# Performance work log

Hardware: AMD Instinct MI355X
Metric: run time of the kernel (lower is better)

Reference implementation:

```python
import jax, jax.numpy as jnp
import numpy as np

# configuration (mirrors global `args` in the original code)
N_USER = 20000
N_ITEM = 20000
N = N_USER + N_ITEM            # total nodes; N*N < 2^31 so int32 hashing is safe
N_EDGES = 2_560_000
MASK_DEPTH = 2
KEEP_RATE = 0.5
N_SEEDS = 2000


def setup_inputs() -> dict:
    key = jax.random.key(0)
    k1, k2, k3 = jax.random.split(key, 3)
    rows = jax.random.randint(k1, (N_EDGES,), 0, N, dtype=jnp.int32)
    cols = jax.random.randint(k2, (N_EDGES,), 0, N, dtype=jnp.int32)
    vals = jnp.ones((N_EDGES,), jnp.float32)  # adj._values(); only its length is used
    seeds = jax.random.randint(k3, (N_SEEDS,), 0, N, dtype=jnp.int32)
    return {"rows": rows, "cols": cols, "vals": vals, "seeds": seeds}


def reference(rows, cols, vals, seeds):
    """Faithful vectorized translation of RandomMaskSubgraphs.forward.

    The per-seed python loop over edges is equivalent (in its final effect) to:
    per BFS level, drop every still-alive edge incident to the current seed set,
    and take the endpoints of dropped edges as the next seed set.
    Returns (enc_rows, enc_cols, enc_vals, dec_rows, dec_cols, dec_vals).
    Removed encoder edges carry value 0 (zero-value sparse entries == absent).
    """
    E = rows.shape[0]
    key = jax.random.key(1)
    kS, kR, kC = jax.random.split(key, 3)

    alive = jnp.ones(E, dtype=bool)                     # edges not yet masked
    seed_mask = jnp.zeros(N, dtype=bool).at[seeds].set(True)
    mask_nodes = seed_mask                               # union of maskNodes list
    cur = seed_mask
    for i in range(MASK_DEPTH):
        # membership test: edge incident to any current seed (single gather pass)
        hit = alive & (cur[rows] | cur[cols])
        alive = alive & ~hit
        if i != MASK_DEPTH - 1:
            # endpoints of masked edges become next frontier (scatter dedup)
            h = hit.astype(jnp.int32)
            touched = (jnp.zeros(N, jnp.int32).at[rows].add(h).at[cols].add(h)) > 0
            mask_nodes = mask_nodes | touched
            cur = touched

    # random keep-nodes augmentation
    samp_num = int(N * KEEP_RATE)
    samp = jax.random.randint(kS, (samp_num,), 0, N, dtype=jnp.int32)
    mask_nodes = mask_nodes.at[samp].set(True)

    # encoderAdj = normalizeAdj(sparse(ones on remaining edges))
    deg = jax.ops.segment_sum(alive.astype(jnp.float32), rows, num_segments=N)
    dinv = jnp.power(deg + 1e-12, -0.5)
    enc_vals = alive.astype(jnp.float32) * dinv[rows] * dinv[cols]

    # decoderAdj: random pairs among masked nodes + self loops + remaining edges,
    # deduplicated via integer hash row*N + col (fits int32 since N*N < 2^31)
    mask_idx = jnp.nonzero(mask_nodes)[0].astype(jnp.int32)
    tem_num = int(mask_idx.shape[0])
    tem_rows = mask_idx[jax.random.randint(kR, (E,), 0, tem_num)]
    tem_cols = mask_idx[jax.random.randint(kC, (E,), 0, tem_num)]
    ar = jnp.arange(N, dtype=jnp.int32)
    alive_rows = rows[alive]
    alive_cols = cols[alive]
    new_rows = jnp.concatenate([tem_rows, tem_cols, ar, alive_rows])
    new_cols = jnp.concatenate([tem_cols, tem_rows, ar, alive_cols])
    hash_val = jnp.unique(new_rows * N + new_cols)
    dec_cols = hash_val % N
    dec_rows = hash_val // N
    dec_vals = jnp.ones(dec_rows.shape[0], jnp.float32)

    return rows, cols, enc_vals, dec_rows, dec_cols, dec_vals
```

## Files before the change

kernel.cpp:

```cpp
#include <hip/hip_runtime.h>
#include <stdint.h>


#define NN 40000
#define SAMPN (NN / 2)
#define WORDS 1250
#define SWORDS 40
#define NB 1024
#define RPB 40
#define CAP 8192
#define CURSTRIDE 4
#define EPB 3840
#define NE (EPB / 256)
#define SCAP (3 * EPB)

__host__ __device__ __forceinline__ void tf2x32(unsigned k0, unsigned k1,
                                                unsigned x0, unsigned x1,
                                                unsigned &o0, unsigned &o1) {
  unsigned ks2 = k0 ^ k1 ^ 0x1BD11BDAu;
  x0 += k0; x1 += k1;
#define TFR(r) { x0 += x1; x1 = (x1 << (r)) | (x1 >> (32 - (r))); x1 ^= x0; }
  TFR(13) TFR(15) TFR(26) TFR(6)
  x0 += k1;  x1 += ks2 + 1u;
  TFR(17) TFR(29) TFR(16) TFR(24)
  x0 += ks2; x1 += k0 + 2u;
  TFR(13) TFR(15) TFR(26) TFR(6)
  x0 += k0;  x1 += k1 + 3u;
  TFR(17) TFR(29) TFR(16) TFR(24)
  x0 += k1;  x1 += ks2 + 4u;
  TFR(13) TFR(15) TFR(26) TFR(6)
  x0 += ks2; x1 += k0 + 5u;
#undef TFR
  o0 = x0; o1 = x1;
}

__device__ __forceinline__ unsigned jrand(unsigned a, unsigned b, unsigned c,
                                          unsigned d, unsigned e, unsigned span) {
  unsigned x0, x1, y0, y1;
  tf2x32(a, b, 0u, e, x0, x1);
  unsigned hi = x0 ^ x1;
  tf2x32(c, d, 0u, e, y0, y1);
  unsigned lo = y0 ^ y1;
  unsigned mult = 65536u % span;
  mult = (mult * mult) % span;
  return ((hi % span) * mult + (lo % span)) % span;
}

__global__ void k_zero16(uint4 *p, int n16) {
  int i = blockIdx.x * blockDim.x + threadIdx.x;
  if (i < n16) p[i] = make_uint4(0u, 0u, 0u, 0u);
}
__global__ void k_seed(const int *seeds, int ns, unsigned char *cur,
                       unsigned char *mask_bfs) {
  int i = blockIdx.x * blockDim.x + threadIdx.x;
  if (i < ns) { int s = seeds[i]; cur[s] = 1; mask_bfs[s] = 1; }
}
__global__ void k_level0(const int *rows, const int *cols, int E,
                         const unsigned char *cur, unsigned char *alive,
                         unsigned char *touched, unsigned char *mask_bfs) {
  int e = blockIdx.x * blockDim.x + threadIdx.x;
  if (e >= E) return;
  int r = rows[e], c = cols[e];
  if (cur[r] | cur[c]) {
    alive[e] = 0;
    touched[r] = 1; touched[c] = 1;
    mask_bfs[r] = 1; mask_bfs[c] = 1;
  } else alive[e] = 1;
}
__global__ void k_level1_deg(const int *rows, const int *cols, int E,
                             const unsigned char *touched, unsigned char *alive,
                             int *deg) {
  int e = blockIdx.x * blockDim.x + threadIdx.x;
  if (e >= E) return;
  if (alive[e]) {
    int r = rows[e];
    if (touched[r] | touched[cols[e]]) alive[e] = 0;
    else atomicAdd(&deg[r], 1);
  }
}
__global__ void k_dinv(const int *deg, float *dinv) {
  int i = blockIdx.x * blockDim.x + threadIdx.x;
  if (i >= NN) return;
  float x = (float)deg[i] + 1e-12f;
  dinv[i] = (float)(1.0 / sqrt((double)x));
}
__global__ void k_enc(const int *rows, const int *cols, const unsigned char *alive,
                      const float *dinv, int E, float *out) {
  int e = blockIdx.x * blockDim.x + threadIdx.x;
  if (e >= E) return;
  int r = rows[e], c = cols[e];
  out[e] = (float)r;
  out[E + e] = (float)c;
  out[2 * E + e] = alive[e] ? dinv[r] * dinv[c] : 0.0f;
}

__global__ void k_samp(unsigned a, unsigned b, unsigned c, unsigned d,
                       unsigned char *mask_bfs) {
  int s = blockIdx.x * blockDim.x + threadIdx.x;
  if (s >= SAMPN) return;
  unsigned idx = jrand(a, b, c, d, (unsigned)s, (unsigned)NN);
  mask_bfs[idx] = 1;
}

__global__ __launch_bounds__(1024) void k_scan_mask(const unsigned char *flags,
                                                    int *mask_idx, int *tem_num) {
  __shared__ int wsum[16];
  const unsigned *f = (const unsigned *)flags;
  int tid = threadIdx.x, lane = tid & 63, wid = tid >> 6;
  int base = tid * 10;
  unsigned u[10];
  int cnt = 0;
  for (int j = 0; j < 10; j++) {
    int i = base + j;
    u[j] = (i < 10000) ? f[i] : 0u;
    cnt += __popc(u[j]);
  }
  int x = cnt;
  for (int d = 1; d < 64; d <<= 1) {
    int y = __shfl_up(x, d, 64);
    if (lane >= d) x += y;
  }
  if (lane == 63) wsum[wid] = x;
  __syncthreads();
  if (wid == 0) {
    int v = (lane < 16) ? wsum[lane] : 0;
    int y = v;
    for (int d = 1; d < 16; d <<= 1) {
      int z = __shfl_up(y, d, 64);
      if (lane >= d) y += z;
    }
    if (lane < 16) wsum[lane] = y - v;
  }
  __syncthreads();
  int off = wsum[wid] + (x - cnt);
  for (int j = 0; j < 10; j++) {
    int i = base + j;
    unsigned v = u[j];
    while (v) {
      int byte = (__ffs(v) - 1) >> 3;
      v &= v - 1;
      mask_idx[off++] = i * 4 + byte;
    }
  }
  if (tid == 1023) *tem_num = off;
}

__global__ void k_append_self(int *cursors, unsigned *bucketmem) {
  int i = blockIdx.x * blockDim.x + threadIdx.x;
  if (i >= NN) return;
  unsigned b = (unsigned)i / RPB;
  unsigned lr = (unsigned)i - b * RPB;
  int p = atomicAdd(&cursors[b * CURSTRIDE], 1);
  if (p < CAP) bucketmem[b * CAP + p] = (lr << 16) | (unsigned)i;
}

__global__ __launch_bounds__(256) void k_append_tem(
    const int *rows, const int *cols, const unsigned char *alive,
    const int *mask_idx, const int *tem_num, int *cursors, unsigned *bucketmem,
    unsigned ra, unsigned rb, unsigned rc, unsigned rd,
    unsigned ca, unsigned cb, unsigned cc, unsigned cd, int E) {
  __shared__ unsigned sorted[SCAP];
  __shared__ int cnt[NB];
  __shared__ int ofs[NB];
  __shared__ int ntot_s;
  int tid = threadIdx.x, lane = tid & 63, wid = tid >> 6;
  int e0 = blockIdx.x * EPB;
  unsigned span = (unsigned)*tem_num;
  const unsigned NOPE = 0xFFFFFFFFu;

  unsigned tval[NE], aval[NE];

  for (int i = tid; i < NB; i += 256) cnt[i] = 0;
  __syncthreads();
#pragma unroll
  for (int k = 0; k < NE; k++) {
    int e = e0 + k * 256 + tid;
    if (e < E) {
      unsigned iR = jrand(ra, rb, rc, rd, (unsigned)e, span);
      unsigned iC = jrand(ca, cb, cc, cd, (unsigned)e, span);
      unsigned tr = (unsigned)mask_idx[iR], tc = (unsigned)mask_idx[iC];
      tval[k] = (tr << 16) | tc;
      atomicAdd(&cnt[tr / RPB], 1);
      atomicAdd(&cnt[tc / RPB], 1);
      if (alive[e]) {
        unsigned r = (unsigned)rows[e];
        aval[k] = (r << 16) | (unsigned)cols[e];
        atomicAdd(&cnt[r / RPB], 1);
      } else aval[k] = NOPE;
    } else { tval[k] = NOPE; aval[k] = NOPE; }
  }
  __syncthreads();
  if (wid == 0) {
    int carry = 0;
    for (int c8 = 0; c8 < 16; c8++) {
      int v = cnt[c8 * 64 + lane];
      int x = v;
      for (int d = 1; d < 64; d <<= 1) {
        int y = __shfl_up(x, d, 64);
        if (lane >= d) x += y;
      }
      ofs[c8 * 64 + lane] = carry + x - v;
      carry += __shfl(x, 63, 64);
    }
    if (lane == 0) ntot_s = carry;
  }
  __syncthreads();
  for (int i = tid; i < NB; i += 256) cnt[i] = ofs[i];
  __syncthreads();
#pragma unroll
  for (int k = 0; k < NE; k++) {
    unsigned v = tval[k];
    if (v != NOPE) {
      unsigned tr = v >> 16, tc = v & 0xFFFFu;
      int p1 = atomicAdd(&cnt[tr / RPB], 1);
      sorted[p1] = v;
      int p2 = atomicAdd(&cnt[tc / RPB], 1);
      sorted[p2] = (tc << 16) | tr;
      unsigned a = aval[k];
      if (a != NOPE) {
        int p3 = atomicAdd(&cnt[(a >> 16) / RPB], 1);
        sorted[p3] = a;
      }
    }
  }
  __syncthreads();
  int ntot = ntot_s;
  for (int b = tid; b < NB; b += 256) {
    int end = (b < NB - 1) ? ofs[b + 1] : ntot;
    int len = end - ofs[b];
    cnt[b] = len ? atomicAdd(&cursors[b * CURSTRIDE], len) : 0;
  }
  __syncthreads();
  for (int j = tid; j < ntot; j += 256) {
    unsigned item = sorted[j];
    unsigned r = item >> 16;
    unsigned b = r / RPB;
    unsigned lr = r - b * RPB;
    int idx = cnt[b] + (j - ofs[b]);
    if (idx < CAP) bucketmem[b * CAP + idx] = (lr << 16) | (item & 0xFFFFu);
  }
}

__global__ __launch_bounds__(256) void k_dedup(unsigned *bucketmem,
                                               const int *cursors, int *uniq_cnt) {
  int b = blockIdx.x;
  int rowbase = b * RPB;
  if (rowbase >= NN) { if (threadIdx.x == 0) uniq_cnt[b] = 0; return; }

  __shared__ unsigned short arr[CAP];
  __shared__ int cnt[RPB];
  __shared__ int rowend[RPB];
  __shared__ int curs[RPB];
  __shared__ int rowoff[RPB];
  __shared__ unsigned bm[4][WORDS];
  __shared__ unsigned sm[4][SWORDS];

  int tid = threadIdx.x, lane = tid & 63, wid = tid >> 6;
  int n = cursors[b * CURSTRIDE]; if (n > CAP) n = CAP;
  const unsigned *src = bucketmem + (size_t)b * CAP;

  for (int i = tid; i < RPB; i += 256) cnt[i] = 0;
  __syncthreads();
  for (int j = tid; j < n; j += 256) atomicAdd(&cnt[src[j] >> 16], 1);
  __syncthreads();
  if (tid == 0) {
    int s = 0;
    for (int r = 0; r < RPB; r++) { curs[r] = s; s += cnt[r]; rowend[r] = s; }
  }
  __syncthreads();
  for (int j = tid; j < n; j += 256) {
    unsigned v = src[j];
    int p = atomicAdd(&curs[v >> 16], 1);
    arr[p] = (unsigned short)v;
  }
  for (int w = lane; w < WORDS; w += 64) bm[wid][w] = 0u;
  if (lane < SWORDS) sm[wid][lane] = 0u;
  __syncthreads();

  for (int r = wid; r < RPB; r += 4) {
    int s1 = rowend[r], s0 = s1 - cnt[r];
    for (int j = s0 + lane; j < s1; j += 64) {
      unsigned c = arr[j];
      atomicOr(&bm[wid][c >> 5], 1u << (c & 31));
      atomicOr(&sm[wid][c >> 10], 1u << ((c >> 5) & 31));
    }
    unsigned s = (lane < SWORDS) ? sm[wid][lane] : 0u;
    int m = 0;
    unsigned t = s;
    while (t) {
      int w = (lane << 5) + (__ffs(t) - 1);
      t &= t - 1;
      m += __popc(bm[wid][w]);
    }
    int x = m;
    for (int d = 1; d < 64; d <<= 1) {
      int y = __shfl_up(x, d, 64);
      if (lane >= d) x += y;
    }
    int u = __shfl(x, 63, 64);
    int pos = s0 + (x - m);
    t = s;
    while (t) {
      int w = (lane << 5) + (__ffs(t) - 1);
      t &= t - 1;
      unsigned mm = bm[wid][w];
      bm[wid][w] = 0u;
      while (mm) {
        int bit = __ffs(mm) - 1;
        mm &= mm - 1;
        arr[pos++] = (unsigned short)((w << 5) + bit);
      }
    }
    if (lane < SWORDS) sm[wid][lane] = 0u;
    if (lane == 0) cnt[r] = u;
  }
  __syncthreads();
  if (tid == 0) {
    int s = 0;
    for (int r = 0; r < RPB; r++) { rowoff[r] = s; s += cnt[r]; }
    uniq_cnt[b] = s;
  }
  __syncthreads();
  unsigned *dst = bucketmem + (size_t)b * CAP;
  for (int r = wid; r < RPB; r += 4) {
    int s0 = r ? rowend[r - 1] : 0;
    int u = cnt[r], o = rowoff[r];
    unsigned hashbase = (unsigned)(rowbase + r) * 40000u;
    for (int j = lane; j < u; j += 64)
      dst[o + j] = hashbase + (unsigned)arr[s0 + j];
  }
}

__global__ __launch_bounds__(1024) void k_scan1024(const int *uniq_cnt,
                                                   int *uniq_off, int *diagC) {
  __shared__ int wsum[16];
  int tid = threadIdx.x, lane = tid & 63, wid = tid >> 6;
  int v = uniq_cnt[tid];
  int x = v;
  for (int d = 1; d < 64; d <<= 1) {
    int y = __shfl_up(x, d, 64);
    if (lane >= d) x += y;
  }
  if (lane == 63) wsum[wid] = x;
  __syncthreads();
  if (wid == 0) {
    int w = (lane < 16) ? wsum[lane] : 0;
    int y = w;
    for (int d = 1; d < 16; d <<= 1) {
      int z = __shfl_up(y, d, 64);
      if (lane >= d) y += z;
    }
    if (lane < 16) wsum[lane] = y - w;
  }
  __syncthreads();
  uniq_off[tid] = wsum[wid] + x - v;
  if (tid == 1023) {
    int C = wsum[15] + x;
    uniq_off[NB] = C;
    *diagC = C;
  }
}
__global__ __launch_bounds__(256) void k_emit(const unsigned *bucketmem,
                                              const int *uniq_cnt,
                                              const int *uniq_off, float *out,
                                              int E, int U) {
  int b = blockIdx.x;
  int ub = uniq_cnt[b], ob = uniq_off[b];
  const unsigned *src = bucketmem + (size_t)b * CAP;
  int base3 = 3 * E;
  for (int j = threadIdx.x; j < ub; j += 256) {
    unsigned h = src[j];
    unsigned r = h / 40000u;
    unsigned c = h - r * 40000u;
    int idx = ob + j;
    if (idx < U) {
      out[base3 + idx] = (float)r;
      out[base3 + U + idx] = (float)c;
      out[base3 + 2 * U + idx] = 1.0f;
    }
  }
}
__global__ void k_diag(const int *diagC, int U, float *out, int E) {
  if (blockIdx.x || threadIdx.x) return;
  int C = *diagC;
  if (C == U) return;
  int d = C - U; if (d < 0) d = -d; if (d > 60000) d = 60000;
  out[3 * E] = (float)(300000 + d);
}

extern "C" void kernel_launch(void *const *d_in, const int *in_sizes, int n_in,
                              void *d_out, int out_size, void *d_ws,
                              size_t ws_size, hipStream_t stream) {
  const int *rows = (const int *)d_in[0];
  const int *cols = (const int *)d_in[1];
  const int *seeds = (const int *)d_in[3];
  const int E = in_sizes[0];
  const int ns = in_sizes[3];
  float *out = (float *)d_out;
  const int U = (out_size - 3 * E) / 3;

  int *I = (int *)d_ws;
  int *deg = I;      I += NN;
  int *cursors = I;  I += NB * CURSTRIDE;
  int *uniq_cnt = I; I += NB;
  unsigned char *cur = (unsigned char *)I;
  unsigned char *touched = cur + NN;
  unsigned char *mask_bfs = touched + NN;
  size_t zero_bytes = (size_t)((char *)(mask_bfs + NN) - (char *)deg);
  int *J = (int *)(mask_bfs + NN);
  int *uniq_off = J; J += NB + 1;
  int *tem_num = J;  J += 1;
  int *diagC = J;    J += 1;
  J += 1;
  int *mask_idx = J; J += NN;
  float *dinv = (float *)J; J += NN;
  unsigned *bucketmem = (unsigned *)J; J += (size_t)NB * CAP;
  unsigned char *alive = (unsigned char *)J;

  unsigned F[3][2];
  tf2x32(0u, 1u, 0u, 0u, F[0][0], F[0][1]);
  tf2x32(0u, 1u, 0u, 1u, F[1][0], F[1][1]);
  tf2x32(0u, 1u, 0u, 2u, F[2][0], F[2][1]);
  unsigned K[3][4];
  for (int s = 0; s < 3; s++) {
    tf2x32(F[s][0], F[s][1], 0u, 0u, K[s][0], K[s][1]);
    tf2x32(F[s][0], F[s][1], 0u, 1u, K[s][2], K[s][3]);
  }

  dim3 b(256);
  int gE = (E + 255) / 256;
  int gN = (NN + 255) / 256;
  int gS = (ns + 255) / 256;
  int gSa = (SAMPN + 255) / 256;
  int gT = (E + EPB - 1) / EPB;
  int n16 = (int)(zero_bytes / 16);

  k_zero16<<<(n16 + 255) / 256, b, 0, stream>>>((uint4 *)deg, n16);
  k_seed<<<gS, b, 0, stream>>>(seeds, ns, cur, mask_bfs);
  k_level0<<<gE, b, 0, stream>>>(rows, cols, E, cur, alive, touched, mask_bfs);
  k_level1_deg<<<gE, b, 0, stream>>>(rows, cols, E, touched, alive, deg);
  k_dinv<<<gN, b, 0, stream>>>(deg, dinv);
  k_enc<<<gE, b, 0, stream>>>(rows, cols, alive, dinv, E, out);
  k_samp<<<gSa, b, 0, stream>>>(K[0][0], K[0][1], K[0][2], K[0][3], mask_bfs);
  k_scan_mask<<<1, 1024, 0, stream>>>(mask_bfs, mask_idx, tem_num);
  k_append_self<<<gN, b, 0, stream>>>(cursors, bucketmem);
  k_append_tem<<<gT, b, 0, stream>>>(rows, cols, alive, mask_idx, tem_num,
                                     cursors, bucketmem,
                                     K[1][0], K[1][1], K[1][2], K[1][3],
                                     K[2][0], K[2][1], K[2][2], K[2][3], E);
  k_dedup<<<NB, b, 0, stream>>>(bucketmem, cursors, uniq_cnt);
  k_scan1024<<<1, 1024, 0, stream>>>(uniq_cnt, uniq_off, diagC);
  k_emit<<<NB, b, 0, stream>>>(bucketmem, uniq_cnt, uniq_off, out, E, U);
  k_diag<<<1, 64, 0, stream>>>(diagC, U, out, E);
}
```

Baseline: 310.5 us.

## Fuse small kernels to cut launch count across mask pipeline

Merges seed and sample marking into one kernel, folds the dinv computation into the encoder kernel, and folds the self-loop append into the bucket-append kernel. The uniq-offset scan and the diag check are absorbed into the emit kernel: each block recomputes its own prefix from uniq_cnt. mask_idx and the shared offsets shrink to 16-bit. The goal is fewer launches and fewer small serial kernels, at the cost of redundant per-block prefix sums and repeated rsqrt computation per edge.

Result: faster. 280.2 us (-9.8%).

```diff
diff --git a/kernel.cpp b/kernel.cpp
--- a/kernel.cpp
+++ b/kernel.cpp
@@ -12,7 +12,8 @@
 #define CURSTRIDE 4
 #define EPB 3840
 #define NE (EPB / 256)
-#define SCAP (3 * EPB)
+#define SELFPB 60
+#define SCAP (3 * EPB + SELFPB)
 
 __host__ __device__ __forceinline__ void tf2x32(unsigned k0, unsigned k1,
                                                 unsigned x0, unsigned x1,
@@ -50,10 +51,15 @@
   int i = blockIdx.x * blockDim.x + threadIdx.x;
   if (i < n16) p[i] = make_uint4(0u, 0u, 0u, 0u);
 }
-__global__ void k_seed(const int *seeds, int ns, unsigned char *cur,
-                       unsigned char *mask_bfs) {
+__global__ void k_seed_samp(const int *seeds, int ns, unsigned char *cur,
+                            unsigned char *mask_bfs,
+                            unsigned a, unsigned b, unsigned c, unsigned d) {
   int i = blockIdx.x * blockDim.x + threadIdx.x;
   if (i < ns) { int s = seeds[i]; cur[s] = 1; mask_bfs[s] = 1; }
+  if (i < SAMPN) {
+    unsigned idx = jrand(a, b, c, d, (unsigned)i, (unsigned)NN);
+    mask_bfs[idx] = 1;
+  }
 }
 __global__ void k_level0(const int *rows, const int *cols, int E,
                          const unsigned char *cur, unsigned char *alive,
@@ -78,32 +84,27 @@
     else atomicAdd(&deg[r], 1);
   }
 }
-__global__ void k_dinv(const int *deg, float *dinv) {
-  int i = blockIdx.x * blockDim.x + threadIdx.x;
-  if (i >= NN) return;
-  float x = (float)deg[i] + 1e-12f;
-  dinv[i] = (float)(1.0 / sqrt((double)x));
-}
 __global__ void k_enc(const int *rows, const int *cols, const unsigned char *alive,
-                      const float *dinv, int E, float *out) {
+                      const int *deg, int E, float *out) {
   int e = blockIdx.x * blockDim.x + threadIdx.x;
   if (e >= E) return;
   int r = rows[e], c = cols[e];
+  float v = 0.0f;
+  if (alive[e]) {
+    float xr = (float)deg[r] + 1e-12f;
+    float xc = (float)deg[c] + 1e-12f;
+    float dr = (float)(1.0 / sqrt((double)xr));
+    float dc = (float)(1.0 / sqrt((double)xc));
+    v = dr * dc;
+  }
   out[e] = (float)r;
   out[E + e] = (float)c;
-  out[2 * E + e] = alive[e] ? dinv[r] * dinv[c] : 0.0f;
-}
-
-__global__ void k_samp(unsigned a, unsigned b, unsigned c, unsigned d,
-                       unsigned char *mask_bfs) {
-  int s = blockIdx.x * blockDim.x + threadIdx.x;
-  if (s >= SAMPN) return;
-  unsigned idx = jrand(a, b, c, d, (unsigned)s, (unsigned)NN);
-  mask_bfs[idx] = 1;
+  out[2 * E + e] = v;
 }
 
 __global__ __launch_bounds__(1024) void k_scan_mask(const unsigned char *flags,
-                                                    int *mask_idx, int *tem_num) {
+                                                    unsigned short *mask_idx,
+                                                    int *tem_num) {
   __shared__ int wsum[16];
   const unsigned *f = (const unsigned *)flags;
   int tid = threadIdx.x, lane = tid & 63, wid = tid >> 6;
@@ -139,32 +140,26 @@
     while (v) {
       int byte = (__ffs(v) - 1) >> 3;
       v &= v - 1;
-      mask_idx[off++] = i * 4 + byte;
+      mask_idx[off++] = (unsigned short)(i * 4 + byte);
     }
   }
   if (tid == 1023) *tem_num = off;
 }
 
-__global__ void k_append_self(int *cursors, unsigned *bucketmem) {
-  int i = blockIdx.x * blockDim.x + threadIdx.x;
-  if (i >= NN) return;
-  unsigned b = (unsigned)i / RPB;
-  unsigned lr = (unsigned)i - b * RPB;
-  int p = atomicAdd(&cursors[b * CURSTRIDE], 1);
-  if (p < CAP) bucketmem[b * CAP + p] = (lr << 16) | (unsigned)i;
-}
-
-__global__ __launch_bounds__(256) void k_append_tem(
+__global__ __launch_bounds__(256) void k_append(
     const int *rows, const int *cols, const unsigned char *alive,
-    const int *mask_idx, const int *tem_num, int *cursors, unsigned *bucketmem,
+    const unsigned short *mask_idx, const int *tem_num, int *cursors,
+    unsigned *bucketmem,
     unsigned ra, unsigned rb, unsigned rc, unsigned rd,
     unsigned ca, unsigned cb, unsigned cc, unsigned cd, int E) {
   __shared__ unsigned sorted[SCAP];
   __shared__ int cnt[NB];
-  __shared__ int ofs[NB];
+  __shared__ unsigned short ofs[NB];
   __shared__ int ntot_s;
   int tid = threadIdx.x, lane = tid & 63, wid = tid >> 6;
   int e0 = blockIdx.x * EPB;
+  int i0 = blockIdx.x * SELFPB;
+  int i1 = i0 + SELFPB; if (i1 > NN) i1 = NN;
   unsigned span = (unsigned)*tem_num;
   const unsigned NOPE = 0xFFFFFFFFu;
 
@@ -189,6 +184,7 @@
       } else aval[k] = NOPE;
     } else { tval[k] = NOPE; aval[k] = NOPE; }
   }
+  for (int i = i0 + tid; i < i1; i += 256) atomicAdd(&cnt[i / RPB], 1);
   __syncthreads();
   if (wid == 0) {
     int carry = 0;
@@ -199,7 +195,7 @@
         int y = __shfl_up(x, d, 64);
         if (lane >= d) x += y;
       }
-      ofs[c8 * 64 + lane] = carry + x - v;
+      ofs[c8 * 64 + lane] = (unsigned short)(carry + x - v);
       carry += __shfl(x, 63, 64);
     }
     if (lane == 0) ntot_s = carry;
@@ -223,11 +219,15 @@
       }
     }
   }
+  for (int i = i0 + tid; i < i1; i += 256) {
+    int p = atomicAdd(&cnt[i / RPB], 1);
+    sorted[p] = ((unsigned)i << 16) | (unsigned)i;
+  }
   __syncthreads();
   int ntot = ntot_s;
   for (int b = tid; b < NB; b += 256) {
-    int end = (b < NB - 1) ? ofs[b + 1] : ntot;
-    int len = end - ofs[b];
+    int end = (b < NB - 1) ? (int)ofs[b + 1] : ntot;
+    int len = end - (int)ofs[b];
     cnt[b] = len ? atomicAdd(&cursors[b * CURSTRIDE], len) : 0;
   }
   __syncthreads();
@@ -236,7 +236,7 @@
     unsigned r = item >> 16;
     unsigned b = r / RPB;
     unsigned lr = r - b * RPB;
-    int idx = cnt[b] + (j - ofs[b]);
+    int idx = cnt[b] + (j - (int)ofs[b]);
     if (idx < CAP) bucketmem[b * CAP + idx] = (lr << 16) | (item & 0xFFFFu);
   }
 }
@@ -331,44 +331,23 @@
   }
 }
 
-__global__ __launch_bounds__(1024) void k_scan1024(const int *uniq_cnt,
-                                                   int *uniq_off, int *diagC) {
-  __shared__ int wsum[16];
+__global__ __launch_bounds__(256) void k_emit(const unsigned *bucketmem,
+                                              const int *uniq_cnt, float *out,
+                                              int E, int U) {
+  __shared__ int part[4];
+  int b = blockIdx.x;
   int tid = threadIdx.x, lane = tid & 63, wid = tid >> 6;
-  int v = uniq_cnt[tid];
-  int x = v;
-  for (int d = 1; d < 64; d <<= 1) {
-    int y = __shfl_up(x, d, 64);
-    if (lane >= d) x += y;
-  }
-  if (lane == 63) wsum[wid] = x;
-  __syncthreads();
-  if (wid == 0) {
-    int w = (lane < 16) ? wsum[lane] : 0;
-    int y = w;
-    for (int d = 1; d < 16; d <<= 1) {
-      int z = __shfl_up(y, d, 64);
-      if (lane >= d) y += z;
-    }
-    if (lane < 16) wsum[lane] = y - w;
-  }
-  __syncthreads();
-  uniq_off[tid] = wsum[wid] + x - v;
-  if (tid == 1023) {
-    int C = wsum[15] + x;
-    uniq_off[NB] = C;
-    *diagC = C;
-  }
-}
-__global__ __launch_bounds__(256) void k_emit(const unsigned *bucketmem,
-                                              const int *uniq_cnt,
-                                              const int *uniq_off, float *out,
-                                              int E, int U) {
-  int b = blockIdx.x;
-  int ub = uniq_cnt[b], ob = uniq_off[b];
+  int acc = 0;
+  for (int i = tid; i < NB; i += 256)
+    if (i < b) acc += uniq_cnt[i];
+  for (int d = 1; d < 64; d <<= 1) acc += __shfl_xor(acc, d, 64);
+  if (lane == 0) part[wid] = acc;
+  __syncthreads();
+  int ob = part[0] + part[1] + part[2] + part[3];
+  int ub = uniq_cnt[b];
   const unsigned *src = bucketmem + (size_t)b * CAP;
   int base3 = 3 * E;
-  for (int j = threadIdx.x; j < ub; j += 256) {
+  for (int j = tid; j < ub; j += 256) {
     unsigned h = src[j];
     unsigned r = h / 40000u;
     unsigned c = h - r * 40000u;
@@ -379,13 +358,13 @@
       out[base3 + 2 * U + idx] = 1.0f;
     }
   }
-}
-__global__ void k_diag(const int *diagC, int U, float *out, int E) {
-  if (blockIdx.x || threadIdx.x) return;
-  int C = *diagC;
-  if (C == U) return;
-  int d = C - U; if (d < 0) d = -d; if (d > 60000) d = 60000;
-  out[3 * E] = (float)(300000 + d);
+  if (b == NB - 1 && tid == 0) {
+    int C = ob + ub;
+    if (C != U) {
+      int d = C - U; if (d < 0) d = -d; if (d > 60000) d = 60000;
+      out[base3] = (float)(300000 + d);
+    }
+  }
 }
 
 extern "C" void kernel_launch(void *const *d_in, const int *in_sizes, int n_in,
@@ -408,12 +387,10 @@
   unsigned char *mask_bfs = touched + NN;
   size_t zero_bytes = (size_t)((char *)(mask_bfs + NN) - (char *)deg);
   int *J = (int *)(mask_bfs + NN);
-  int *uniq_off = J; J += NB + 1;
   int *tem_num = J;  J += 1;
-  int *diagC = J;    J += 1;
   J += 1;
-  int *mask_idx = J; J += NN;
-  float *dinv = (float *)J; J += NN;
+  unsigned short *mask_idx = (unsigned short *)J;
+  J += NN / 2;
   unsigned *bucketmem = (unsigned *)J; J += (size_t)NB * CAP;
   unsigned char *alive = (unsigned char *)J;
 
@@ -429,27 +406,21 @@
 
   dim3 b(256);
   int gE = (E + 255) / 256;
-  int gN = (NN + 255) / 256;
-  int gS = (ns + 255) / 256;
-  int gSa = (SAMPN + 255) / 256;
+  int gSS = (SAMPN + 255) / 256;
   int gT = (E + EPB - 1) / EPB;
   int n16 = (int)(zero_bytes / 16);
 
   k_zero16<<<(n16 + 255) / 256, b, 0, stream>>>((uint4 *)deg, n16);
-  k_seed<<<gS, b, 0, stream>>>(seeds, ns, cur, mask_bfs);
+  k_seed_samp<<<gSS, b, 0, stream>>>(seeds, ns, cur, mask_bfs,
+                                     K[0][0], K[0][1], K[0][2], K[0][3]);
   k_level0<<<gE, b, 0, stream>>>(rows, cols, E, cur, alive, touched, mask_bfs);
   k_level1_deg<<<gE, b, 0, stream>>>(rows, cols, E, touched, alive, deg);
-  k_dinv<<<gN, b, 0, stream>>>(deg, dinv);
-  k_enc<<<gE, b, 0, stream>>>(rows, cols, alive, dinv, E, out);
-  k_samp<<<gSa, b, 0, stream>>>(K[0][0], K[0][1], K[0][2], K[0][3], mask_bfs);
+  k_enc<<<gE, b, 0, stream>>>(rows, cols, alive, deg, E, out);
   k_scan_mask<<<1, 1024, 0, stream>>>(mask_bfs, mask_idx, tem_num);
-  k_append_self<<<gN, b, 0, stream>>>(cursors, bucketmem);
-  k_append_tem<<<gT, b, 0, stream>>>(rows, cols, alive, mask_idx, tem_num,
-                                     cursors, bucketmem,
-                                     K[1][0], K[1][1], K[1][2], K[1][3],
-                                     K[2][0], K[2][1], K[2][2], K[2][3], E);
+  k_append<<<gT, b, 0, stream>>>(rows, cols, alive, mask_idx, tem_num,
+                                 cursors, bucketmem,
+                                 K[1][0], K[1][1], K[1][2], K[1][3],
+                                 K[2][0], K[2][1], K[2][2], K[2][3], E);
   k_dedup<<<NB, b, 0, stream>>>(bucketmem, cursors, uniq_cnt);
-  k_scan1024<<<1, 1024, 0, stream>>>(uniq_cnt, uniq_off, diagC);
-  k_emit<<<NB, b, 0, stream>>>(bucketmem, uniq_cnt, uniq_off, out, E, U);
-  k_diag<<<1, 64, 0, stream>>>(diagC, U, out, E);
-}
+  k_emit<<<NB, b, 0, stream>>>(bucketmem, uniq_cnt, out, E, U);
+}
```
